# Kernel optimization log

Hardware: AMD Instinct MI355X
Metric: run time of the kernel (lower is better)

## Reference

```python
import jax, jax.numpy as jnp
import numpy as np

N, IN_DIM, LDIM = 8192, 512, 256
NEG_SLOPE = 0.01  # torch F.leaky_relu default
EPS = 1e-10


def setup_inputs() -> dict:
    key = jax.random.key(0)
    k1, k2, k3, k4 = jax.random.split(key, 4)
    x = jax.random.normal(k1, (N, IN_DIM), dtype=jnp.float32)
    adj = jax.random.uniform(k2, (N, N), dtype=jnp.float32)
    # nn.Linear(in_dim, learning_dim, bias=False) weight: [learning_dim, in_dim]
    proj_w = jax.random.normal(k3, (LDIM, IN_DIM), dtype=jnp.float32) * (1.0 / np.sqrt(IN_DIM))
    # nn.init.uniform_(learn_w, a=0, b=1)
    learn_w = jax.random.uniform(k4, (LDIM,), dtype=jnp.float32)
    return {"x": x, "adj": adj, "proj_w": proj_w, "learn_w": learn_w}


def reference(x, adj, proj_w, learn_w):
    # x_hat = projection(x): [N, LDIM]
    x_hat = x @ proj_w.T
    # cosine-distance score: sum_d w_d * (1 - xn_i[d] * xn_j[d])
    #   = sum(w) - (xn * w) @ xn.T  -- avoids the N x N x D intermediate
    xn = x_hat / jnp.linalg.norm(x_hat, axis=-1, keepdims=True)  # [N, LDIM]
    scores = jnp.sum(learn_w) - jnp.einsum('id,jd->ij', xn * learn_w, xn)  # [N, N]
    out = jax.nn.leaky_relu(scores, NEG_SLOPE)
    out = out - jnp.max(out, axis=-1, keepdims=True)
    soft_adj = adj * jnp.exp(out)
    soft_adj = soft_adj / jnp.sum(soft_adj, axis=-1, keepdims=True) + EPS
    return soft_adj
```

## Files before the change

### kernel.cpp

```cpp
#include <hip/hip_runtime.h>
#include <stdint.h>

#define NN 8192
#define KDIM 512
#define LDIM 256

typedef short bf16x8 __attribute__((ext_vector_type(8)));
typedef short short8 __attribute__((ext_vector_type(8)));
typedef float f32x4 __attribute__((ext_vector_type(4)));

__device__ __forceinline__ unsigned short f2bf(float f) {
  unsigned int u = __float_as_uint(f);
  u = (u + 0x7fffu + ((u >> 16) & 1u)) >> 16;
  return (unsigned short)u;
}
__device__ __forceinline__ float bf2f(unsigned short s) {
  return __uint_as_float(((unsigned int)s) << 16);
}

__device__ __forceinline__ void async_ld16(const unsigned short* g, unsigned short* l) {
  __builtin_amdgcn_global_load_lds(
      (const __attribute__((address_space(1))) unsigned int*)g,
      (__attribute__((address_space(3))) unsigned int*)l, 16, 0, 0);
}

__global__ __launch_bounds__(256) void cast_kernel(
    const float* __restrict__ x, const float* __restrict__ pw,
    unsigned short* __restrict__ xb, unsigned short* __restrict__ pwb) {
  int i = blockIdx.x * 256 + threadIdx.x;
  xb[i] = f2bf(x[i]);
  if (i < LDIM * KDIM) pwb[i] = f2bf(pw[i]);
}

__global__ __launch_bounds__(256) void norm_kernel(
    const float* __restrict__ xh, const float* __restrict__ w,
    unsigned short* __restrict__ Ab, unsigned short* __restrict__ Bb) {
  const int row = blockIdx.x;
  const int d = threadIdx.x;
  const float v = xh[row * LDIM + d];
  float ss = v * v;
#pragma unroll
  for (int m = 1; m < 64; m <<= 1) ss += __shfl_xor(ss, m);
  __shared__ float s4[4];
  if ((d & 63) == 0) s4[d >> 6] = ss;
  __syncthreads();
  const float tot = s4[0] + s4[1] + s4[2] + s4[3];
  const float inv = 1.0f / sqrtf(tot);
  const float xn = v * inv;
  Bb[row * LDIM + d] = f2bf(xn);
  Ab[row * LDIM + d] = f2bf(xn * w[d]);
}

template <int K, int MODE>
__global__ __launch_bounds__(256) void gemm_bt(
    const unsigned short* __restrict__ A,
    const unsigned short* __restrict__ B,
    float* __restrict__ C,
    unsigned short* __restrict__ T,
    const float* __restrict__ adj,
    float* __restrict__ rowsum,
    int ldC) {
  __shared__ unsigned short As[128 * 32];
  __shared__ unsigned short Bs[128 * 32];
  __shared__ float rs[128];

  const int tid = threadIdx.x;
  const int wave = tid >> 6;
  const int lane = tid & 63;
  const int quad = lane >> 4;
  const int l16 = lane & 15;
  const int wm = wave >> 1;
  const int wn = wave & 1;

  const size_t row0 = (size_t)blockIdx.y * 128;
  const size_t col0 = (size_t)blockIdx.x * 128;

  const int c0 = wave * 128 + lane;
  const int mA = c0 >> 2;
  const int kA = (c0 & 3) * 8;
  const unsigned short* Ag = A + (row0 + mA) * (size_t)K + kA;
  const unsigned short* Bg = B + (col0 + mA) * (size_t)K + kA;
  char* AsB = (char*)As;
  char* BsB = (char*)Bs;
  unsigned short* dA0 = (unsigned short*)(AsB + wave * 2048);
  unsigned short* dA1 = (unsigned short*)(AsB + wave * 2048 + 1024);
  unsigned short* dB0 = (unsigned short*)(BsB + wave * 2048);
  unsigned short* dB1 = (unsigned short*)(BsB + wave * 2048 + 1024);

  f32x4 acc[4][4];
#pragma unroll
  for (int i = 0; i < 4; ++i)
#pragma unroll
    for (int j = 0; j < 4; ++j) acc[i][j] = (f32x4)(0.0f);

  for (int k0 = 0; k0 < K; k0 += 32) {
    async_ld16(Ag + k0, dA0);
    async_ld16(Ag + 16 * (size_t)K + k0, dA1);
    async_ld16(Bg + k0, dB0);
    async_ld16(Bg + 16 * (size_t)K + k0, dB1);
    __syncthreads();

    bf16x8 av[4], bv[4];
#pragma unroll
    for (int mt = 0; mt < 4; ++mt)
      av[mt] = *(const bf16x8*)(AsB + (wm * 64 + mt * 16 + l16) * 64 + quad * 16);
#pragma unroll
    for (int nt = 0; nt < 4; ++nt)
      bv[nt] = *(const bf16x8*)(BsB + (wn * 64 + nt * 16 + l16) * 64 + quad * 16);
#pragma unroll
    for (int mt = 0; mt < 4; ++mt)
#pragma unroll
      for (int nt = 0; nt < 4; ++nt)
        acc[mt][nt] = __builtin_amdgcn_mfma_f32_16x16x32_bf16(av[mt], bv[nt], acc[mt][nt], 0, 0, 0);
    __syncthreads();
  }

  if constexpr (MODE == 0) {
#pragma unroll
    for (int mt = 0; mt < 4; ++mt)
#pragma unroll
      for (int nt = 0; nt < 4; ++nt)
#pragma unroll
        for (int r = 0; r < 4; ++r) {
          size_t gr = row0 + wm * 64 + mt * 16 + quad * 4 + r;
          size_t gc = col0 + wn * 64 + nt * 16 + l16;
          C[gr * (size_t)ldC + gc] = acc[mt][nt][r];
        }
  } else {
    __shared__ float trans[32 * 132];
    const int s = tid >> 3;
    const int cb = tid & 7;
    const int coff = cb * 16;
#pragma unroll
    for (int mt = 0; mt < 4; ++mt) {
      __syncthreads();
#pragma unroll
      for (int nt = 0; nt < 4; ++nt)
#pragma unroll
        for (int r = 0; r < 4; ++r)
          trans[(wm * 16 + quad * 4 + r) * 132 + wn * 64 + nt * 16 + l16] =
              acc[mt][nt][r];
      __syncthreads();
      const size_t gr = row0 + (size_t)(s >> 4) * 64 + mt * 16 + (s & 15);
      const float* arow = adj + gr * NN + col0 + coff;
      float av16[16];
#pragma unroll
      for (int q = 0; q < 4; ++q) {
        float4 a4 = ((const float4*)arow)[q];
        av16[q * 4 + 0] = a4.x;
        av16[q * 4 + 1] = a4.y;
        av16[q * 4 + 2] = a4.z;
        av16[q * 4 + 3] = a4.w;
      }
      const float* drow = &trans[s * 132 + coff];
      float part = 0.0f;
      if constexpr (MODE == 1) {
        short8 p0, p1;
#pragma unroll
        for (int j = 0; j < 16; ++j) {
          float tv = av16[j] * __expf(-drow[j]);
          unsigned short us = f2bf(tv);
          part += bf2f(us);
          if (j < 8) p0[j] = (short)us; else p1[j - 8] = (short)us;
        }
        short8* trow = (short8*)(T + gr * NN + col0 + coff);
        trow[0] = p0;
        trow[1] = p1;
      } else {
        float4 o[4];
#pragma unroll
        for (int j = 0; j < 16; ++j) {
          float tv = av16[j] * __expf(-drow[j]);
          part += tv;
          ((float*)o)[j] = tv;
        }
        float4* crow = (float4*)(C + gr * NN + col0 + coff);
#pragma unroll
        for (int q = 0; q < 4; ++q) crow[q] = o[q];
      }
      part += __shfl_xor(part, 1);
      part += __shfl_xor(part, 2);
      part += __shfl_xor(part, 4);
      if (cb == 0) rs[(s >> 4) * 64 + mt * 16 + (s & 15)] = part;
    }
    __syncthreads();
    if (tid < 128) atomicAdd(&rowsum[row0 + tid], rs[tid]);
  }
}

__global__ __launch_bounds__(256) void scale_bf16_kernel(
    const unsigned short* __restrict__ T, const float* __restrict__ rowsum,
    float* __restrict__ out) {
  const size_t i = (size_t)blockIdx.x * 256 + threadIdx.x;
  const int row = (int)(i >> 10);
  short8 tv = ((const short8*)T)[i];
  const float inv = 1.0f / rowsum[row];
  float4 o0, o1;
  o0.x = bf2f((unsigned short)tv[0]) * inv + 1e-10f;
  o0.y = bf2f((unsigned short)tv[1]) * inv + 1e-10f;
  o0.z = bf2f((unsigned short)tv[2]) * inv + 1e-10f;
  o0.w = bf2f((unsigned short)tv[3]) * inv + 1e-10f;
  o1.x = bf2f((unsigned short)tv[4]) * inv + 1e-10f;
  o1.y = bf2f((unsigned short)tv[5]) * inv + 1e-10f;
  o1.z = bf2f((unsigned short)tv[6]) * inv + 1e-10f;
  o1.w = bf2f((unsigned short)tv[7]) * inv + 1e-10f;
  ((float4*)out)[i * 2] = o0;
  ((float4*)out)[i * 2 + 1] = o1;
}

__global__ __launch_bounds__(256) void scale_f32_kernel(
    float* __restrict__ t, const float* __restrict__ rowsum) {
  const size_t i = (size_t)blockIdx.x * 256 + threadIdx.x;
  const int row = (int)(i >> 11);
  float4 v = ((float4*)t)[i];
  const float inv = 1.0f / rowsum[row];
  v.x = v.x * inv + 1e-10f;
  v.y = v.y * inv + 1e-10f;
  v.z = v.z * inv + 1e-10f;
  v.w = v.w * inv + 1e-10f;
  ((float4*)t)[i] = v;
}

extern "C" void kernel_launch(void* const* d_in, const int* in_sizes, int n_in,
                              void* d_out, int out_size, void* d_ws, size_t ws_size,
                              hipStream_t stream) {
  (void)in_sizes; (void)n_in; (void)out_size;
  const float* x   = (const float*)d_in[0];
  const float* adj = (const float*)d_in[1];
  const float* pw  = (const float*)d_in[2];
  const float* lw  = (const float*)d_in[3];
  float* out = (float*)d_out;
  char* ws = (char*)d_ws;

  unsigned short* xb   = (unsigned short*)(ws);
  unsigned short* pwb  = (unsigned short*)(ws + 8388608);
  float*          xhat = (float*)(ws + 8650752);
  unsigned short* Ab   = (unsigned short*)(ws + 17039360);
  unsigned short* Bb   = (unsigned short*)(ws + 21233664);
  float*          rsum = (float*)(ws + 25427968);
  unsigned short* Tbuf = (unsigned short*)(ws + 25460736);
  const bool big_ws = ws_size >= 25460736ull + (size_t)NN * NN * 2ull;

  cast_kernel<<<(NN * KDIM) / 256, 256, 0, stream>>>(x, pw, xb, pwb);
  gemm_bt<KDIM, 0><<<dim3(2, 64), 256, 0, stream>>>(xb, pwb, xhat, nullptr, nullptr, nullptr, LDIM);
  norm_kernel<<<NN, 256, 0, stream>>>(xhat, lw, Ab, Bb);
  hipMemsetAsync(rsum, 0, NN * sizeof(float), stream);
  if (big_ws) {
    gemm_bt<LDIM, 1><<<dim3(64, 64), 256, 0, stream>>>(Ab, Bb, nullptr, Tbuf, adj, rsum, NN);
    scale_bf16_kernel<<<(NN / 8) * (NN / 256), 256, 0, stream>>>(Tbuf, rsum, out);
  } else {
    gemm_bt<LDIM, 2><<<dim3(64, 64), 256, 0, stream>>>(Ab, Bb, out, nullptr, adj, rsum, NN);
    scale_f32_kernel<<<(NN / 4) * (NN / 256), 256, 0, stream>>>(out, rsum);
  }
}
```

Measured before the change: 542.9 us.

## Double-buffer GEMM LDS, restructure epilogue, vectorize cast and scale kernels

```diff
diff --git a/kernel.cpp b/kernel.cpp
--- a/kernel.cpp
+++ b/kernel.cpp
@@ -8,6 +8,7 @@
 typedef short bf16x8 __attribute__((ext_vector_type(8)));
 typedef short short8 __attribute__((ext_vector_type(8)));
 typedef float f32x4 __attribute__((ext_vector_type(4)));
+typedef unsigned short u16x4 __attribute__((ext_vector_type(4)));
 
 __device__ __forceinline__ unsigned short f2bf(float f) {
   unsigned int u = __float_as_uint(f);
@@ -18,7 +19,7 @@
   return __uint_as_float(((unsigned int)s) << 16);
 }
 
-__device__ __forceinline__ void async_ld16(const unsigned short* g, unsigned short* l) {
+__device__ __forceinline__ void async_ld16(const unsigned short* g, void* l) {
   __builtin_amdgcn_global_load_lds(
       (const __attribute__((address_space(1))) unsigned int*)g,
       (__attribute__((address_space(3))) unsigned int*)l, 16, 0, 0);
@@ -27,9 +28,19 @@
 __global__ __launch_bounds__(256) void cast_kernel(
     const float* __restrict__ x, const float* __restrict__ pw,
     unsigned short* __restrict__ xb, unsigned short* __restrict__ pwb) {
-  int i = blockIdx.x * 256 + threadIdx.x;
-  xb[i] = f2bf(x[i]);
-  if (i < LDIM * KDIM) pwb[i] = f2bf(pw[i]);
+  const int i = blockIdx.x * 256 + threadIdx.x;
+  float4 v = ((const float4*)x)[i];
+  u16x4 o;
+  o[0] = (short)f2bf(v.x); o[1] = (short)f2bf(v.y);
+  o[2] = (short)f2bf(v.z); o[3] = (short)f2bf(v.w);
+  ((u16x4*)xb)[i] = o;
+  if (i < (LDIM * KDIM) / 4) {
+    float4 w = ((const float4*)pw)[i];
+    u16x4 ow;
+    ow[0] = (short)f2bf(w.x); ow[1] = (short)f2bf(w.y);
+    ow[2] = (short)f2bf(w.z); ow[3] = (short)f2bf(w.w);
+    ((u16x4*)pwb)[i] = ow;
+  }
 }
 
 __global__ __launch_bounds__(256) void norm_kernel(
@@ -60,8 +71,8 @@
     const float* __restrict__ adj,
     float* __restrict__ rowsum,
     int ldC) {
-  __shared__ unsigned short As[128 * 32];
-  __shared__ unsigned short Bs[128 * 32];
+  constexpr int SMEM_BYTES = (MODE == 0) ? 32768 : 128 * 132 * 4;
+  __shared__ alignas(16) char sm[SMEM_BYTES];
   __shared__ float rs[128];
 
   const int tid = threadIdx.x;
@@ -80,12 +91,11 @@
   const int kA = (c0 & 3) * 8;
   const unsigned short* Ag = A + (row0 + mA) * (size_t)K + kA;
   const unsigned short* Bg = B + (col0 + mA) * (size_t)K + kA;
-  char* AsB = (char*)As;
-  char* BsB = (char*)Bs;
-  unsigned short* dA0 = (unsigned short*)(AsB + wave * 2048);
-  unsigned short* dA1 = (unsigned short*)(AsB + wave * 2048 + 1024);
-  unsigned short* dB0 = (unsigned short*)(BsB + wave * 2048);
-  unsigned short* dB1 = (unsigned short*)(BsB + wave * 2048 + 1024);
+
+  char* const a0d = sm + wave * 2048;
+  char* const b0d = sm + 8192 + wave * 2048;
+  char* const a1d = sm + 16384 + wave * 2048;
+  char* const b1d = sm + 24576 + wave * 2048;
 
   f32x4 acc[4][4];
 #pragma unroll
@@ -93,25 +103,36 @@
 #pragma unroll
     for (int j = 0; j < 4; ++j) acc[i][j] = (f32x4)(0.0f);
 
-  for (int k0 = 0; k0 < K; k0 += 32) {
-    async_ld16(Ag + k0, dA0);
-    async_ld16(Ag + 16 * (size_t)K + k0, dA1);
-    async_ld16(Bg + k0, dB0);
-    async_ld16(Bg + 16 * (size_t)K + k0, dB1);
-    __syncthreads();
-
+  auto stage = [&](char* Ad, char* Bd, int k0) {
+    async_ld16(Ag + k0, Ad);
+    async_ld16(Ag + 16 * (size_t)K + k0, Ad + 1024);
+    async_ld16(Bg + k0, Bd);
+    async_ld16(Bg + 16 * (size_t)K + k0, Bd + 1024);
+  };
+  auto compute = [&](const char* Ab_, const char* Bb_) {
     bf16x8 av[4], bv[4];
 #pragma unroll
     for (int mt = 0; mt < 4; ++mt)
-      av[mt] = *(const bf16x8*)(AsB + (wm * 64 + mt * 16 + l16) * 64 + quad * 16);
+      av[mt] = *(const bf16x8*)(Ab_ + (wm * 64 + mt * 16 + l16) * 64 + quad * 16);
 #pragma unroll
     for (int nt = 0; nt < 4; ++nt)
-      bv[nt] = *(const bf16x8*)(BsB + (wn * 64 + nt * 16 + l16) * 64 + quad * 16);
+      bv[nt] = *(const bf16x8*)(Bb_ + (wn * 64 + nt * 16 + l16) * 64 + quad * 16);
 #pragma unroll
     for (int mt = 0; mt < 4; ++mt)
 #pragma unroll
       for (int nt = 0; nt < 4; ++nt)
-        acc[mt][nt] = __builtin_amdgcn_mfma_f32_16x16x32_bf16(av[mt], bv[nt], acc[mt][nt], 0, 0, 0);
+        acc[mt][nt] = __builtin_amdgcn_mfma_f32_16x16x32_bf16(
+            av[mt], bv[nt], acc[mt][nt], 0, 0, 0);
+  };
+
+  stage(a0d, b0d, 0);
+  __syncthreads();
+  for (int k0 = 0; k0 < K; k0 += 64) {
+    if (k0 + 32 < K) stage(a1d, b1d, k0 + 32);
+    compute(sm, sm + 8192);
+    __syncthreads();
+    if (k0 + 64 < K) stage(a0d, b0d, k0 + 64);
+    if (k0 + 32 < K) compute(sm + 16384, sm + 24576);
     __syncthreads();
   }
 
@@ -127,62 +148,65 @@
           C[gr * (size_t)ldC + gc] = acc[mt][nt][r];
         }
   } else {
-    __shared__ float trans[32 * 132];
-    const int s = tid >> 3;
-    const int cb = tid & 7;
-    const int coff = cb * 16;
-#pragma unroll
-    for (int mt = 0; mt < 4; ++mt) {
-      __syncthreads();
+    float* trans = (float*)sm;
+#pragma unroll
+    for (int mt = 0; mt < 4; ++mt)
 #pragma unroll
       for (int nt = 0; nt < 4; ++nt)
 #pragma unroll
         for (int r = 0; r < 4; ++r)
-          trans[(wm * 16 + quad * 4 + r) * 132 + wn * 64 + nt * 16 + l16] =
-              acc[mt][nt][r];
-      __syncthreads();
-      const size_t gr = row0 + (size_t)(s >> 4) * 64 + mt * 16 + (s & 15);
-      const float* arow = adj + gr * NN + col0 + coff;
-      float av16[16];
+          trans[(wm * 64 + mt * 16 + quad * 4 + r) * 132 +
+                wn * 64 + nt * 16 + l16] = acc[mt][nt][r];
+    __syncthreads();
+
+    const int r16 = tid >> 1;
+    const int h = tid & 1;
+    const size_t gr = row0 + r16;
+    const float4* arow = (const float4*)(adj + gr * NN + col0 + h * 64);
+    const float4* drow = (const float4*)(trans + r16 * 132 + h * 64);
+    f32x4 ps = (f32x4)(0.0f);
+#pragma unroll
+    for (int g = 0; g < 4; ++g) {
+      float4 a4[4], d4[4];
 #pragma unroll
       for (int q = 0; q < 4; ++q) {
-        float4 a4 = ((const float4*)arow)[q];
-        av16[q * 4 + 0] = a4.x;
-        av16[q * 4 + 1] = a4.y;
-        av16[q * 4 + 2] = a4.z;
-        av16[q * 4 + 3] = a4.w;
+        a4[q] = arow[g * 4 + q];
+        d4[q] = drow[g * 4 + q];
       }
-      const float* drow = &trans[s * 132 + coff];
-      float part = 0.0f;
+      float tv[16];
+#pragma unroll
+      for (int q = 0; q < 4; ++q) {
+        tv[q * 4 + 0] = a4[q].x * __expf(-d4[q].x);
+        tv[q * 4 + 1] = a4[q].y * __expf(-d4[q].y);
+        tv[q * 4 + 2] = a4[q].z * __expf(-d4[q].z);
+        tv[q * 4 + 3] = a4[q].w * __expf(-d4[q].w);
+      }
       if constexpr (MODE == 1) {
         short8 p0, p1;
 #pragma unroll
         for (int j = 0; j < 16; ++j) {
-          float tv = av16[j] * __expf(-drow[j]);
-          unsigned short us = f2bf(tv);
-          part += bf2f(us);
+          unsigned short us = f2bf(tv[j]);
+          ps[j & 3] += bf2f(us);
           if (j < 8) p0[j] = (short)us; else p1[j - 8] = (short)us;
         }
-        short8* trow = (short8*)(T + gr * NN + col0 + coff);
+        short8* trow = (short8*)(T + gr * NN + col0 + h * 64 + g * 16);
         trow[0] = p0;
         trow[1] = p1;
       } else {
         float4 o[4];
 #pragma unroll
         for (int j = 0; j < 16; ++j) {
-          float tv = av16[j] * __expf(-drow[j]);
-          part += tv;
-          ((float*)o)[j] = tv;
+          ps[j & 3] += tv[j];
+          ((float*)o)[j] = tv[j];
         }
-        float4* crow = (float4*)(C + gr * NN + col0 + coff);
+        float4* crow = (float4*)(C + gr * NN + col0 + h * 64 + g * 16);
 #pragma unroll
         for (int q = 0; q < 4; ++q) crow[q] = o[q];
       }
-      part += __shfl_xor(part, 1);
-      part += __shfl_xor(part, 2);
-      part += __shfl_xor(part, 4);
-      if (cb == 0) rs[(s >> 4) * 64 + mt * 16 + (s & 15)] = part;
     }
+    float part = ps[0] + ps[1] + ps[2] + ps[3];
+    part += __shfl_xor(part, 1);
+    if (h == 0) rs[r16] = part;
     __syncthreads();
     if (tid < 128) atomicAdd(&rowsum[row0 + tid], rs[tid]);
   }
@@ -192,20 +216,29 @@
     const unsigned short* __restrict__ T, const float* __restrict__ rowsum,
     float* __restrict__ out) {
   const size_t i = (size_t)blockIdx.x * 256 + threadIdx.x;
-  const int row = (int)(i >> 10);
-  short8 tv = ((const short8*)T)[i];
+  const int row = (int)(i >> 9);
   const float inv = 1.0f / rowsum[row];
-  float4 o0, o1;
-  o0.x = bf2f((unsigned short)tv[0]) * inv + 1e-10f;
-  o0.y = bf2f((unsigned short)tv[1]) * inv + 1e-10f;
-  o0.z = bf2f((unsigned short)tv[2]) * inv + 1e-10f;
-  o0.w = bf2f((unsigned short)tv[3]) * inv + 1e-10f;
-  o1.x = bf2f((unsigned short)tv[4]) * inv + 1e-10f;
-  o1.y = bf2f((unsigned short)tv[5]) * inv + 1e-10f;
-  o1.z = bf2f((unsigned short)tv[6]) * inv + 1e-10f;
-  o1.w = bf2f((unsigned short)tv[7]) * inv + 1e-10f;
-  ((float4*)out)[i * 2] = o0;
-  ((float4*)out)[i * 2 + 1] = o1;
+  short8 t0 = ((const short8*)T)[i * 2];
+  short8 t1 = ((const short8*)T)[i * 2 + 1];
+  float4 o0, o1, o2, o3;
+  o0.x = bf2f((unsigned short)t0[0]) * inv + 1e-10f;
+  o0.y = bf2f((unsigned short)t0[1]) * inv + 1e-10f;
+  o0.z = bf2f((unsigned short)t0[2]) * inv + 1e-10f;
+  o0.w = bf2f((unsigned short)t0[3]) * inv + 1e-10f;
+  o1.x = bf2f((unsigned short)t0[4]) * inv + 1e-10f;
+  o1.y = bf2f((unsigned short)t0[5]) * inv + 1e-10f;
+  o1.z = bf2f((unsigned short)t0[6]) * inv + 1e-10f;
+  o1.w = bf2f((unsigned short)t0[7]) * inv + 1e-10f;
+  o2.x = bf2f((unsigned short)t1[0]) * inv + 1e-10f;
+  o2.y = bf2f((unsigned short)t1[1]) * inv + 1e-10f;
+  o2.z = bf2f((unsigned short)t1[2]) * inv + 1e-10f;
+  o2.w = bf2f((unsigned short)t1[3]) * inv + 1e-10f;
+  o3.x = bf2f((unsigned short)t1[4]) * inv + 1e-10f;
+  o3.y = bf2f((unsigned short)t1[5]) * inv + 1e-10f;
+  o3.z = bf2f((unsigned short)t1[6]) * inv + 1e-10f;
+  o3.w = bf2f((unsigned short)t1[7]) * inv + 1e-10f;
+  float4* dst = (float4*)(out + i * 16);
+  dst[0] = o0; dst[1] = o1; dst[2] = o2; dst[3] = o3;
 }
 
 __global__ __launch_bounds__(256) void scale_f32_kernel(
@@ -241,13 +274,13 @@
   unsigned short* Tbuf = (unsigned short*)(ws + 25460736);
   const bool big_ws = ws_size >= 25460736ull + (size_t)NN * NN * 2ull;
 
-  cast_kernel<<<(NN * KDIM) / 256, 256, 0, stream>>>(x, pw, xb, pwb);
+  cast_kernel<<<(NN * KDIM) / (256 * 4), 256, 0, stream>>>(x, pw, xb, pwb);
   gemm_bt<KDIM, 0><<<dim3(2, 64), 256, 0, stream>>>(xb, pwb, xhat, nullptr, nullptr, nullptr, LDIM);
   norm_kernel<<<NN, 256, 0, stream>>>(xhat, lw, Ab, Bb);
   hipMemsetAsync(rsum, 0, NN * sizeof(float), stream);
   if (big_ws) {
     gemm_bt<LDIM, 1><<<dim3(64, 64), 256, 0, stream>>>(Ab, Bb, nullptr, Tbuf, adj, rsum, NN);
-    scale_bf16_kernel<<<(NN / 8) * (NN / 256), 256, 0, stream>>>(Tbuf, rsum, out);
+    scale_bf16_kernel<<<(NN * NN) / (16 * 256), 256, 0, stream>>>(Tbuf, rsum, out);
   } else {
     gemm_bt<LDIM, 2><<<dim3(64, 64), 256, 0, stream>>>(Ab, Bb, out, nullptr, adj, rsum, NN);
     scale_f32_kernel<<<(NN / 4) * (NN / 256), 256, 0, stream>>>(out, rsum);
```

New measurement: 612.8 us. 12.9% more time.
